# Kernel optimization log

Hardware: AMD Instinct MI355X
Metric: run time of the kernel (lower is better)

The kernel has to match this reference:

```python
import jax, jax.numpy as jnp
import numpy as np

B, T, C, HS = 512, 256, 256, 64

def setup_inputs() -> dict:
    key = jax.random.key(0)
    kx, kq, kk, kv = jax.random.split(key, 4)
    x = jax.random.normal(kx, (B, T, C), dtype=jnp.float32)
    # nn.Linear(n_embd, head_size, bias=False): store as [in, out] for x @ W
    Wq = jax.random.normal(kq, (C, HS), dtype=jnp.float32) * (C ** -0.5)
    Wk = jax.random.normal(kk, (C, HS), dtype=jnp.float32) * (C ** -0.5)
    Wv = jax.random.normal(kv, (C, HS), dtype=jnp.float32) * (C ** -0.5)
    return {"x": x, "Wq": Wq, "Wk": Wk, "Wv": Wv}

def reference(x, Wq, Wk, Wv):
    # self-attention path (key_input/value_input are None)
    q = x @ Wq  # [B, T, HS]
    k = x @ Wk
    v = x @ Wv
    # NOTE: original scales by C**-0.5 (full embed dim), not head_size**-0.5
    wei = jnp.einsum('bqd,bkd->bqk', q, k) * (C ** -0.5)  # [B, T, T]
    Tq = x.shape[1]
    causal = jnp.tril(jnp.ones((Tq, Tq), dtype=bool))
    wei = jnp.where(causal, wei, -jnp.inf)
    wei = jax.nn.softmax(wei, axis=-1)
    # dropout p=0 -> identity
    out = wei @ v  # [B, T, HS]
    return out
```

## Files before the change

### kernel.cpp

```cpp
#include <hip/hip_runtime.h>
#include <hip/hip_bf16.h>
#include <cstdint>
#include <cmath>

#define B_ 512
#define T_ 256
#define C_ 256
#define HS_ 64

typedef short bf16x8 __attribute__((ext_vector_type(8)));
typedef float f32x4 __attribute__((ext_vector_type(4)));

static __device__ __forceinline__ unsigned short f2bf(float f) {
    union { float f; unsigned int u; } v; v.f = f;
    unsigned int r = v.u + 0x7fffu + ((v.u >> 16) & 1u);
    return (unsigned short)(r >> 16);
}

static __device__ __forceinline__ uint2 pack4(f32x4 a) {
    uint2 r;
    r.x = (unsigned)f2bf(a[0]) | ((unsigned)f2bf(a[1]) << 16);
    r.y = (unsigned)f2bf(a[2]) | ((unsigned)f2bf(a[3]) << 16);
    return r;
}

#define VKEY(vr) ((((vr) & 7) << 4) + (((vr) & 8) << 2))

__global__ void wt_kernel(const float* __restrict__ Wq, const float* __restrict__ Wk,
                          const float* __restrict__ Wv, unsigned short* __restrict__ WTf) {
    int idx = blockIdx.x * 256 + threadIdx.x;
    if (idx >= 96 * 64) return;
    int fb = idx >> 6;
    int l = idx & 63;
    int ws = fb >> 5;
    int rem = fb & 31;
    int f = rem >> 3;
    int kap = rem & 7;
    const float* W = (ws == 0) ? Wq : ((ws == 1) ? Wk : Wv);
    unsigned short o[8];
#pragma unroll
    for (int j = 0; j < 8; ++j) {
        int k = kap * 32 + (l >> 4) * 8 + j;
        int n = f * 16 + (l & 15);
        o[j] = f2bf(W[k * HS_ + n]);
    }
    *(ulonglong2*)(WTf + (size_t)idx * 8) = *(ulonglong2*)o;
}

__global__ __launch_bounds__(512)
__attribute__((amdgpu_num_vgpr(128)))
void fused_kernel(const float* __restrict__ x, const unsigned short* __restrict__ WTf,
                  float* __restrict__ out) {
    __shared__ __align__(16) char smem[81920];
    unsigned short* Ks  = (unsigned short*)(smem);
    unsigned short* Vts = (unsigned short*)(smem + 32768);
    char* xbuf = smem + 65536;

    const int tid = threadIdx.x;
    const int w = tid >> 6, l = tid & 63, ln = l & 15, lg = l >> 4;
    const int b = blockIdx.x;
    const float* xb = x + (size_t)b * (T_ * C_);
    const int qt = w >> 2, qf = w & 3;
    const float scale = 0.0625f;

    float4 st[4];

#define LOADX(S) do { \
    _Pragma("unroll") \
    for (int i_ = 0; i_ < 4; ++i_) \
        st[i_] = *(const float4*)(xb + (S) * 8192 + (size_t)(i_ * 512 + tid) * 4); \
} while (0)

#define DS_WRITE_SLAB() do { \
    _Pragma("unroll") \
    for (int i_ = 0; i_ < 4; ++i_) { \
        const int fidx_ = i_ * 512 + tid, row_ = fidx_ >> 6, c4_ = (fidx_ & 63) * 4; \
        ushort4 hh_; \
        hh_.x = f2bf(st[i_].x); hh_.y = f2bf(st[i_].y); \
        hh_.z = f2bf(st[i_].z); hh_.w = f2bf(st[i_].w); \
        *(ushort4*)(xbuf + row_ * 512 + ((c4_ * 2) ^ ((row_ & 7) << 4))) = hh_; \
    } \
} while (0)

    bf16x8 bkv[8], bq[8];
#pragma unroll
    for (int kap = 0; kap < 8; ++kap) {
        bkv[kap] = *(const bf16x8*)(WTf + ((size_t)((4 + w) * 8 + kap) * 64 + l) * 8);
        bq[kap]  = *(const bf16x8*)(WTf + ((size_t)(qf * 8 + kap) * 64 + l) * 8);
    }

    uint2 hqQ[8];

    LOADX(0);
#pragma unroll
    for (int s = 0; s < 8; ++s) {
        DS_WRITE_SLAB();
        __syncthreads();
        if (s < 7) LOADX(s + 1);

        f32x4 aq   = (f32x4){0.f, 0.f, 0.f, 0.f};
        f32x4 akv0 = (f32x4){0.f, 0.f, 0.f, 0.f};
        f32x4 akv1 = (f32x4){0.f, 0.f, 0.f, 0.f};
#pragma unroll
        for (int kap = 0; kap < 8; ++kap) {
            bf16x8 a0 = *(const bf16x8*)(xbuf + ln * 512
                          + ((kap * 64 + lg * 16) ^ ((ln & 7) << 4)));
            const int R1 = 16 + ln;
            bf16x8 a1 = *(const bf16x8*)(xbuf + R1 * 512
                          + ((kap * 64 + lg * 16) ^ ((R1 & 7) << 4)));
            akv0 = __builtin_amdgcn_mfma_f32_16x16x32_bf16(bkv[kap], a0, akv0, 0, 0, 0);
            akv1 = __builtin_amdgcn_mfma_f32_16x16x32_bf16(bkv[kap], a1, akv1, 0, 0, 0);
            aq   = __builtin_amdgcn_mfma_f32_16x16x32_bf16(bq[kap], qt ? a1 : a0, aq, 0, 0, 0);
        }
        hqQ[s] = pack4(aq);

        if (w < 4) {
#pragma unroll
            for (int tt = 0; tt < 2; ++tt) {
                const int token = s * 32 + tt * 16 + ln;
                uint2 hv = pack4(tt ? akv1 : akv0);
                *(uint2*)((char*)Ks + token * 128
                          + ((w * 32 + lg * 8) ^ ((token & 7) << 4))) = hv;
            }
        } else {
#pragma unroll
            for (int tt = 0; tt < 2; ++tt) {
                const int token = s * 32 + tt * 16 + ln;
                f32x4 av = tt ? akv1 : akv0;
#pragma unroll
                for (int i = 0; i < 4; ++i) {
                    const int vr = (w - 4) * 16 + lg * 4 + i;
                    *(unsigned short*)((char*)Vts + vr * 512
                          + ((token * 2) ^ VKEY(vr))) = f2bf(av[i]);
                }
            }
        }
        __syncthreads();
    }

    bf16x8 qa0[2], qa1[2];
#pragma unroll
    for (int s = 0; s < 4; ++s) {
        const int row = s * 32 + qt * 16 + ln;
        *(uint2*)(xbuf + row * 128 + ((qf * 32 + lg * 8) ^ ((row & 7) << 4))) = hqQ[s];
    }
    __syncthreads();
#pragma unroll
    for (int kk = 0; kk < 2; ++kk) {
        const int row = w * 16 + ln;
        qa0[kk] = *(const bf16x8*)(xbuf + row * 128
                    + ((kk * 64 + lg * 16) ^ ((row & 7) << 4)));
    }
    __syncthreads();
#pragma unroll
    for (int s = 4; s < 8; ++s) {
        const int row = (s - 4) * 32 + qt * 16 + ln;
        *(uint2*)(xbuf + row * 128 + ((qf * 32 + lg * 8) ^ ((row & 7) << 4))) = hqQ[s];
    }
    __syncthreads();
#pragma unroll
    for (int kk = 0; kk < 2; ++kk) {
        const int row = (7 - w) * 16 + ln;
        qa1[kk] = *(const bf16x8*)(xbuf + row * 128
                    + ((kk * 64 + lg * 16) ^ ((row & 7) << 4)));
    }
    __syncthreads();

    unsigned short* Pl = (unsigned short*)(xbuf + w * 1280);
    float* outb = out + (size_t)b * (T_ * HS_);

#pragma unroll
    for (int pass = 0; pass < 2; ++pass) {
        const int g = pass ? (15 - w) : w;
        const int r0 = g * 16;
        const int qrow = r0 + ln;

        float m = -INFINITY, lsum = 0.f;
        f32x4 o[4];
#pragma unroll
        for (int f = 0; f < 4; ++f) o[f] = (f32x4){0.f, 0.f, 0.f, 0.f};

        const int nkt = (g >> 1) + 1;
        for (int kt = 0; kt < nkt; ++kt) {
            const int n0 = kt * 32;

            f32x4 s2[2];
            __builtin_amdgcn_s_setprio(1);
#pragma unroll
            for (int h = 0; h < 2; ++h) {
                const int key = n0 + 16 * h + ln;
                bf16x8 kb0 = *(const bf16x8*)((char*)Ks + key * 128
                               + ((lg * 16) ^ ((key & 7) << 4)));
                bf16x8 kb1 = *(const bf16x8*)((char*)Ks + key * 128
                               + ((64 + lg * 16) ^ ((key & 7) << 4)));
                f32x4 z = (f32x4){0.f, 0.f, 0.f, 0.f};
                z = __builtin_amdgcn_mfma_f32_16x16x32_bf16(kb0, pass ? qa1[0] : qa0[0], z, 0, 0, 0);
                s2[h] = __builtin_amdgcn_mfma_f32_16x16x32_bf16(kb1, pass ? qa1[1] : qa0[1], z, 0, 0, 0);
            }
            __builtin_amdgcn_s_setprio(0);

            float sm[2][4];
#pragma unroll
            for (int h = 0; h < 2; ++h)
#pragma unroll
                for (int r = 0; r < 4; ++r) {
                    const int key = n0 + 16 * h + lg * 4 + r;
                    float v = s2[h][r] * scale;
                    sm[h][r] = (qrow >= key) ? v : -INFINITY;
                }

            float tmax = fmaxf(fmaxf(fmaxf(sm[0][0], sm[0][1]), fmaxf(sm[0][2], sm[0][3])),
                               fmaxf(fmaxf(sm[1][0], sm[1][1]), fmaxf(sm[1][2], sm[1][3])));
            tmax = fmaxf(tmax, __shfl_xor(tmax, 16, 64));
            tmax = fmaxf(tmax, __shfl_xor(tmax, 32, 64));

            if (!__all(tmax <= m)) {
                const float mn = fmaxf(m, tmax);
                const float fac = __expf(m - mn);
                lsum *= fac;
                m = mn;
#pragma unroll
                for (int f = 0; f < 4; ++f) o[f] *= fac;
            }

            float p[2][4];
            float rs = 0.f;
#pragma unroll
            for (int h = 0; h < 2; ++h)
#pragma unroll
                for (int r = 0; r < 4; ++r) {
                    p[h][r] = __expf(sm[h][r] - m);
                    rs += p[h][r];
                }
            rs += __shfl_xor(rs, 16, 64);
            rs += __shfl_xor(rs, 32, 64);
            lsum += rs;

#pragma unroll
            for (int h = 0; h < 2; ++h)
#pragma unroll
                for (int rp = 0; rp < 2; ++rp) {
                    unsigned pk = (unsigned)f2bf(p[h][2 * rp])
                                | ((unsigned)f2bf(p[h][2 * rp + 1]) << 16);
                    *(unsigned*)(Pl + ln * 40 + 16 * h + lg * 4 + 2 * rp) = pk;
                }

            bf16x8 pa = *(const bf16x8*)(Pl + ln * 40 + lg * 8);

            __builtin_amdgcn_s_setprio(1);
#pragma unroll
            for (int f = 0; f < 4; ++f) {
                const int vr = f * 16 + ln;
                bf16x8 vb = *(const bf16x8*)((char*)Vts + vr * 512
                              + ((n0 * 2 + lg * 16) ^ VKEY(vr)));
                o[f] = __builtin_amdgcn_mfma_f32_16x16x32_bf16(vb, pa, o[f], 0, 0, 0);
            }
            __builtin_amdgcn_s_setprio(0);
        }

        const float inv = 1.f / lsum;
#pragma unroll
        for (int f = 0; f < 4; ++f) {
            float4 sv;
            sv.x = o[f][0] * inv; sv.y = o[f][1] * inv;
            sv.z = o[f][2] * inv; sv.w = o[f][3] * inv;
            *(float4*)(outb + (size_t)qrow * HS_ + f * 16 + lg * 4) = sv;
        }
    }
}

extern "C" void kernel_launch(void* const* d_in, const int* in_sizes, int n_in,
                              void* d_out, int out_size, void* d_ws, size_t ws_size,
                              hipStream_t stream) {
    const float* x  = (const float*)d_in[0];
    const float* Wq = (const float*)d_in[1];
    const float* Wk = (const float*)d_in[2];
    const float* Wv = (const float*)d_in[3];
    float* out = (float*)d_out;

    unsigned short* WTf = (unsigned short*)d_ws;

    wt_kernel<<<24, 256, 0, stream>>>(Wq, Wk, Wv, WTf);
    fused_kernel<<<B_, 512, 0, stream>>>(x, WTf, out);
}
```

Before: 51.98 us.

## Software-pipeline QK^T MFMA for next key tile over current softmax

Measured after the change: 52.51 us. Within noise of the previous version (+1.0%).

```diff
diff --git a/kernel.cpp b/kernel.cpp
--- a/kernel.cpp
+++ b/kernel.cpp
@@ -169,11 +169,87 @@
     unsigned short* Pl = (unsigned short*)(xbuf + w * 1280);
     float* outb = out + (size_t)b * (T_ * HS_);
 
+#define QKT(N0, S2, QAv) do { \
+    __builtin_amdgcn_s_setprio(1); \
+    _Pragma("unroll") \
+    for (int h_ = 0; h_ < 2; ++h_) { \
+        const int key_ = (N0) + 16 * h_ + ln; \
+        bf16x8 kb0_ = *(const bf16x8*)((char*)Ks + key_ * 128 \
+                        + ((lg * 16) ^ ((key_ & 7) << 4))); \
+        bf16x8 kb1_ = *(const bf16x8*)((char*)Ks + key_ * 128 \
+                        + ((64 + lg * 16) ^ ((key_ & 7) << 4))); \
+        f32x4 z_ = (f32x4){0.f, 0.f, 0.f, 0.f}; \
+        z_ = __builtin_amdgcn_mfma_f32_16x16x32_bf16(kb0_, QAv[0], z_, 0, 0, 0); \
+        S2[h_] = __builtin_amdgcn_mfma_f32_16x16x32_bf16(kb1_, QAv[1], z_, 0, 0, 0); \
+    } \
+    __builtin_amdgcn_s_setprio(0); \
+} while (0)
+
+#define KTBODY(SCUR, SNXT, QAv) do { \
+    const int n0 = kt * 32; \
+    float sm[2][4]; \
+    _Pragma("unroll") \
+    for (int h_ = 0; h_ < 2; ++h_) \
+        _Pragma("unroll") \
+        for (int r_ = 0; r_ < 4; ++r_) { \
+            const int key_ = n0 + 16 * h_ + lg * 4 + r_; \
+            float v_ = SCUR[h_][r_] * scale; \
+            sm[h_][r_] = (qrow >= key_) ? v_ : -INFINITY; \
+        } \
+    if (kt + 1 < nkt) QKT((kt + 1) * 32, SNXT, QAv);    \
+    float tmax = fmaxf(fmaxf(fmaxf(sm[0][0], sm[0][1]), fmaxf(sm[0][2], sm[0][3])), \
+                       fmaxf(fmaxf(sm[1][0], sm[1][1]), fmaxf(sm[1][2], sm[1][3]))); \
+    tmax = fmaxf(tmax, __shfl_xor(tmax, 16, 64)); \
+    tmax = fmaxf(tmax, __shfl_xor(tmax, 32, 64)); \
+    if (!__all(tmax <= m)) { \
+        const float mn = fmaxf(m, tmax); \
+        const float fac = __expf(m - mn); \
+        lsum *= fac; \
+        m = mn; \
+        _Pragma("unroll") \
+        for (int f_ = 0; f_ < 4; ++f_) o[f_] *= fac; \
+    } \
+    float p_[2][4]; \
+    float rs = 0.f; \
+    _Pragma("unroll") \
+    for (int h_ = 0; h_ < 2; ++h_) \
+        _Pragma("unroll") \
+        for (int r_ = 0; r_ < 4; ++r_) { \
+            p_[h_][r_] = __expf(sm[h_][r_] - m); \
+            rs += p_[h_][r_]; \
+        } \
+    rs += __shfl_xor(rs, 16, 64); \
+    rs += __shfl_xor(rs, 32, 64); \
+    lsum += rs; \
+    _Pragma("unroll") \
+    for (int h_ = 0; h_ < 2; ++h_) \
+        _Pragma("unroll") \
+        for (int rp_ = 0; rp_ < 2; ++rp_) { \
+            unsigned pk_ = (unsigned)f2bf(p_[h_][2 * rp_]) \
+                         | ((unsigned)f2bf(p_[h_][2 * rp_ + 1]) << 16); \
+            *(unsigned*)(Pl + ln * 40 + 16 * h_ + lg * 4 + 2 * rp_) = pk_; \
+        } \
+    bf16x8 pa_ = *(const bf16x8*)(Pl + ln * 40 + lg * 8); \
+    __builtin_amdgcn_s_setprio(1); \
+    _Pragma("unroll") \
+    for (int f_ = 0; f_ < 4; ++f_) { \
+        const int vr_ = f_ * 16 + ln; \
+        bf16x8 vb_ = *(const bf16x8*)((char*)Vts + vr_ * 512 \
+                       + ((n0 * 2 + lg * 16) ^ VKEY(vr_))); \
+        o[f_] = __builtin_amdgcn_mfma_f32_16x16x32_bf16(vb_, pa_, o[f_], 0, 0, 0); \
+    } \
+    __builtin_amdgcn_s_setprio(0); \
+    ++kt; \
+} while (0)
+
 #pragma unroll
     for (int pass = 0; pass < 2; ++pass) {
         const int g = pass ? (15 - w) : w;
         const int r0 = g * 16;
         const int qrow = r0 + ln;
+        bf16x8 qav[2];
+        qav[0] = pass ? qa1[0] : qa0[0];
+        qav[1] = pass ? qa1[1] : qa0[1];
 
         float m = -INFINITY, lsum = 0.f;
         f32x4 o[4];
@@ -181,81 +257,13 @@
         for (int f = 0; f < 4; ++f) o[f] = (f32x4){0.f, 0.f, 0.f, 0.f};
 
         const int nkt = (g >> 1) + 1;
-        for (int kt = 0; kt < nkt; ++kt) {
-            const int n0 = kt * 32;
-
-            f32x4 s2[2];
-            __builtin_amdgcn_s_setprio(1);
-#pragma unroll
-            for (int h = 0; h < 2; ++h) {
-                const int key = n0 + 16 * h + ln;
-                bf16x8 kb0 = *(const bf16x8*)((char*)Ks + key * 128
-                               + ((lg * 16) ^ ((key & 7) << 4)));
-                bf16x8 kb1 = *(const bf16x8*)((char*)Ks + key * 128
-                               + ((64 + lg * 16) ^ ((key & 7) << 4)));
-                f32x4 z = (f32x4){0.f, 0.f, 0.f, 0.f};
-                z = __builtin_amdgcn_mfma_f32_16x16x32_bf16(kb0, pass ? qa1[0] : qa0[0], z, 0, 0, 0);
-                s2[h] = __builtin_amdgcn_mfma_f32_16x16x32_bf16(kb1, pass ? qa1[1] : qa0[1], z, 0, 0, 0);
-            }
-            __builtin_amdgcn_s_setprio(0);
-
-            float sm[2][4];
-#pragma unroll
-            for (int h = 0; h < 2; ++h)
-#pragma unroll
-                for (int r = 0; r < 4; ++r) {
-                    const int key = n0 + 16 * h + lg * 4 + r;
-                    float v = s2[h][r] * scale;
-                    sm[h][r] = (qrow >= key) ? v : -INFINITY;
-                }
-
-            float tmax = fmaxf(fmaxf(fmaxf(sm[0][0], sm[0][1]), fmaxf(sm[0][2], sm[0][3])),
-                               fmaxf(fmaxf(sm[1][0], sm[1][1]), fmaxf(sm[1][2], sm[1][3])));
-            tmax = fmaxf(tmax, __shfl_xor(tmax, 16, 64));
-            tmax = fmaxf(tmax, __shfl_xor(tmax, 32, 64));
-
-            if (!__all(tmax <= m)) {
-                const float mn = fmaxf(m, tmax);
-                const float fac = __expf(m - mn);
-                lsum *= fac;
-                m = mn;
-#pragma unroll
-                for (int f = 0; f < 4; ++f) o[f] *= fac;
-            }
-
-            float p[2][4];
-            float rs = 0.f;
-#pragma unroll
-            for (int h = 0; h < 2; ++h)
-#pragma unroll
-                for (int r = 0; r < 4; ++r) {
-                    p[h][r] = __expf(sm[h][r] - m);
-                    rs += p[h][r];
-                }
-            rs += __shfl_xor(rs, 16, 64);
-            rs += __shfl_xor(rs, 32, 64);
-            lsum += rs;
-
-#pragma unroll
-            for (int h = 0; h < 2; ++h)
-#pragma unroll
-                for (int rp = 0; rp < 2; ++rp) {
-                    unsigned pk = (unsigned)f2bf(p[h][2 * rp])
-                                | ((unsigned)f2bf(p[h][2 * rp + 1]) << 16);
-                    *(unsigned*)(Pl + ln * 40 + 16 * h + lg * 4 + 2 * rp) = pk;
-                }
-
-            bf16x8 pa = *(const bf16x8*)(Pl + ln * 40 + lg * 8);
-
-            __builtin_amdgcn_s_setprio(1);
-#pragma unroll
-            for (int f = 0; f < 4; ++f) {
-                const int vr = f * 16 + ln;
-                bf16x8 vb = *(const bf16x8*)((char*)Vts + vr * 512
-                              + ((n0 * 2 + lg * 16) ^ VKEY(vr)));
-                o[f] = __builtin_amdgcn_mfma_f32_16x16x32_bf16(vb, pa, o[f], 0, 0, 0);
-            }
-            __builtin_amdgcn_s_setprio(0);
+        f32x4 sA[2], sB[2];
+        int kt = 0;
+        QKT(0, sA, qav);
+        while (kt < nkt) {
+            KTBODY(sA, sB, qav);
+            if (kt >= nkt) break;
+            KTBODY(sB, sA, qav);
         }
 
         const float inv = 1.f / lsum;
```
